# Kernel optimization log

Hardware: AMD Instinct MI355X
Metric: run time of the kernel (lower is better)

Reference implementation:

```python
import jax, jax.numpy as jnp
import numpy as np

B, T, H = 2, 2048, 1024
NH = 16
D = H // NH  # head_dim = 64
SCALE = D ** -0.5


def setup_inputs() -> dict:
    key = jax.random.key(0)
    ks = jax.random.split(key, 10)
    s_in = 1.0 / np.sqrt(H)   # torch Linear init scale for fan_in=H
    s_d = 1.0 / np.sqrt(D)
    return {
        "x":  jax.random.normal(ks[0], (B, T, H), jnp.float32),
        # stacked per-head Q/K projections: [NH, H, D] weights, [NH, D] biases
        "Wq": jax.random.uniform(ks[1], (NH, H, D), jnp.float32, -s_in, s_in),
        "bq": jax.random.uniform(ks[2], (NH, D), jnp.float32, -s_in, s_in),
        "Wk": jax.random.uniform(ks[3], (NH, H, D), jnp.float32, -s_in, s_in),
        "bk": jax.random.uniform(ks[4], (NH, D), jnp.float32, -s_in, s_in),
        # shared V projection H->D
        "Wv": jax.random.uniform(ks[5], (H, D), jnp.float32, -s_in, s_in),
        "bv": jax.random.uniform(ks[6], (D,), jnp.float32, -s_in, s_in),
        # out projection D->H
        "Wo": jax.random.uniform(ks[7], (D, H), jnp.float32, -s_d, s_d),
        "bo": jax.random.uniform(ks[8], (H,), jnp.float32, -s_d, s_d),
    }


def reference(x, Wq, bq, Wk, bk, Wv, bv, Wo, bo):
    # shared value projection: [B,T,D]
    v = jnp.einsum('bth,hd->btd', x, Wv) + bv
    # batched per-head Q/K projections: [NH,B,T,D]
    q = jnp.einsum('bth,nhd->nbtd', x, Wq) + bq[:, None, None, :]
    k = jnp.einsum('bth,nhd->nbtd', x, Wk) + bk[:, None, None, :]
    # scaled causal attention scores: [NH,B,T,T]
    scores = jnp.einsum('nbtd,nbsd->nbts', q, k) * SCALE
    causal = jnp.triu(jnp.ones((T, T), bool), k=1)  # True above diagonal
    scores = jnp.where(causal, -jnp.inf, scores)
    weights = jax.nn.softmax(scores, axis=-1)  # dropout is identity in eval
    # shared V attended per head, then mean over heads: [B,T,D]
    mean_head = jnp.einsum('nbts,bsd->btd', weights, v) / NH
    out = jnp.einsum('btd,dh->bth', mean_head, Wo) + bo
    mean_weights = jnp.mean(weights, axis=0)  # [B,T,T]
    return out, mean_weights
```

## Files before the change

kernel.cpp:

```cpp
#include <hip/hip_runtime.h>
#include <hip/hip_bf16.h>

#define B_ 2
#define T_ 2048
#define H_ 1024
#define NH_ 16
#define D_ 64
#define BT_ (B_*T_)
#define SCALE_ 0.125f
#define LOG2E_ 1.4426950408889634f

typedef _Float16 f16x8 __attribute__((ext_vector_type(8)));
typedef float f32x4 __attribute__((ext_vector_type(4)));

#define MFMA(a,b,c) __builtin_amdgcn_mfma_f32_16x16x32_f16((a),(b),(c),0,0,0)
#define EXP2(x) __builtin_amdgcn_exp2f(x)

typedef const __attribute__((address_space(1))) void GV;
typedef __attribute__((address_space(3))) void LV;

__device__ __forceinline__ size_t toff(int r, int c, int C) {
    return (size_t)((r >> 4) * (C >> 5) + (c >> 5)) * 512 + (size_t)(((c & 31) >> 3) * 128 + (r & 15) * 8 + (c & 7));
}
__device__ __forceinline__ f16x8 frag_ld(const _Float16* base, int rt, int kc, int Cc, int l15, int quad) {
    return *(const f16x8*)(base + (size_t)(rt * Cc + kc) * 512 + quad * 128 + l15 * 8);
}
__device__ __forceinline__ int fbase(int p) {
    int m = p >> 1;
    return (p & 1) ? (m + 1) * (m + 1) : m * m + m;
}

__global__ __launch_bounds__(256) void k_prep(const float* __restrict__ x,
                                              const float* __restrict__ Wq, const float* __restrict__ Wk,
                                              const float* __restrict__ Wv, const float* __restrict__ Wo,
                                              _Float16* __restrict__ xb, _Float16* __restrict__ wqk,
                                              _Float16* __restrict__ wvt, _Float16* __restrict__ wot,
                                              float* __restrict__ mw) {
    int blk = blockIdx.x, tid = threadIdx.x;
    if (blk < 256) {
        const float* xs = x + ((size_t)blk << 14);
        _Float16* dstb = xb + ((size_t)blk << 14);
#pragma unroll
        for (int it = 0; it < 8; it++) {
            int E = it * 2048 + tid * 8;
            int rr = (E >> 3) & 15;
            int h = (E >> 9) * 32 + ((E >> 7) & 3) * 8;
            const float* p = xs + (size_t)rr * 1024 + h;
            float4 f0 = *(const float4*)p;
            float4 f1 = *(const float4*)(p + 4);
            f16x8 o;
            o[0]=(_Float16)f0.x; o[1]=(_Float16)f0.y; o[2]=(_Float16)f0.z; o[3]=(_Float16)f0.w;
            o[4]=(_Float16)f1.x; o[5]=(_Float16)f1.y; o[6]=(_Float16)f1.z; o[7]=(_Float16)f1.w;
            *(f16x8*)(dstb + E) = o;
        }
    } else if (blk < 384) {
        int ct = blk - 256;
        const float* W = (ct < 64) ? Wq : Wk;
        int head = (ct >> 2) & 15;
        int dbase = (ct & 3) * 16;
        _Float16* dstb = wqk + ((size_t)ct << 14);
#pragma unroll
        for (int it = 0; it < 8; it++) {
            int E = it * 2048 + tid * 8;
            int rr = (E >> 3) & 15;
            int h = (E >> 9) * 32 + ((E >> 7) & 3) * 8;
            const float* src = W + (size_t)head * 65536 + (size_t)h * 64 + dbase + rr;
            f16x8 o;
#pragma unroll
            for (int e = 0; e < 8; e++) o[e] = (_Float16)src[(size_t)e * 64];
            *(f16x8*)(dstb + E) = o;
        }
    } else if (blk < 388) {
        int rt = blk - 384;
        _Float16* dstb = wvt + ((size_t)rt << 14);
#pragma unroll
        for (int it = 0; it < 8; it++) {
            int E = it * 2048 + tid * 8;
            int rr = (E >> 3) & 15;
            int h = (E >> 9) * 32 + ((E >> 7) & 3) * 8;
            const float* src = Wv + (size_t)h * 64 + rt * 16 + rr;
            f16x8 o;
#pragma unroll
            for (int e = 0; e < 8; e++) o[e] = (_Float16)src[(size_t)e * 64];
            *(f16x8*)(dstb + E) = o;
        }
    } else if (blk < 392) {
        int bl = blk - 388;
#pragma unroll
        for (int it = 0; it < 8; it++) {
            int G = bl * 16384 + it * 2048 + tid * 8;
            int rt = G >> 10;
            int rem = G & 1023;
            int rr = (rem >> 3) & 15;
            int dd = (rem >> 9) * 32 + ((rem >> 7) & 3) * 8;
            const float* src = Wo + (size_t)dd * 1024 + rt * 16 + rr;
            f16x8 o;
#pragma unroll
            for (int e = 0; e < 8; e++) o[e] = (_Float16)src[(size_t)e * 1024];
            *(f16x8*)(wot + G) = o;
        }
    } else {
        int iz = blk - 392;
        int b = (iz >= 496) ? 1 : 0;
        int i = iz - b * 496;
        int s64 = (int)((sqrtf(8.f * i + 1.f) + 1.f) * 0.5f);
        if (s64 * (s64 - 1) / 2 > i) s64--;
        if ((s64 + 1) * s64 / 2 <= i) s64++;
        int q64 = i - s64 * (s64 - 1) / 2;
        float4 z = {0.f, 0.f, 0.f, 0.f};
#pragma unroll
        for (int it = 0; it < 4; it++) {
            int idx = it * 256 + tid;
            int r = idx >> 4, c4 = idx & 15;
            *(float4*)&mw[(size_t)(b * T_ + q64 * 64 + r) * T_ + s64 * 64 + c4 * 4] = z;
        }
    }
}

__global__ __launch_bounds__(256) void k_gemm(const _Float16* __restrict__ xb, const _Float16* __restrict__ wqk,
                                              const float* __restrict__ bq, const float* __restrict__ bk,
                                              const _Float16* __restrict__ wvt, const float* __restrict__ bv,
                                              _Float16* __restrict__ qh, _Float16* __restrict__ kh,
                                              _Float16* __restrict__ vt) {
    __shared__ __align__(16) unsigned char smem[32768];
    _Float16* As = (_Float16*)smem;
    _Float16* Bs = (_Float16*)(smem + 16384);
    int tid = threadIdx.x, w = tid >> 6, lane = tid & 63, l15 = lane & 15, quad = lane >> 4;
    if (blockIdx.x >= 512) {
        float (*red)[16][64] = (float(*)[16][64])smem;
        int rt = blockIdx.x - 512;
        f32x4 acc[4];
#pragma unroll
        for (int j = 0; j < 4; j++) acc[j] = (f32x4){0.f, 0.f, 0.f, 0.f};
        for (int q = 0; q < 8; q++) {
            int kc = w * 8 + q;
            f16x8 a = frag_ld(xb, rt, kc, 32, l15, quad);
#pragma unroll
            for (int j = 0; j < 4; j++) {
                f16x8 bb = frag_ld(wvt, j, kc, 32, l15, quad);
                acc[j] = MFMA(a, bb, acc[j]);
            }
        }
#pragma unroll
        for (int j = 0; j < 4; j++)
#pragma unroll
            for (int r = 0; r < 4; r++) red[w][quad * 4 + r][j * 16 + l15] = acc[j][r];
        __syncthreads();
        int r = tid >> 4, dg = tid & 15;
        int b = rt >> 7, tt = (rt & 127) * 16 + r;
        _Float16* vtb = vt + (size_t)b * 131072;
#pragma unroll
        for (int e = 0; e < 4; e++) {
            int d = dg * 4 + e;
            float s = red[0][r][d] + red[1][r][d] + red[2][r][d] + red[3][r][d] + bv[d];
            vtb[toff(d, tt, 2048)] = (_Float16)s;
        }
        return;
    }
    int bm = blockIdx.x >> 4, bn = blockIdx.x & 15;
    int rowbase = (w >> 1) * 64, colbase = (w & 1) * 64;
    f32x4 acc[4][4];
#pragma unroll
    for (int i = 0; i < 4; i++)
#pragma unroll
        for (int j = 0; j < 4; j++) acc[i][j] = (f32x4){0.f, 0.f, 0.f, 0.f};

    for (int kk = 0; kk < 16; kk++) {
        __syncthreads();
#pragma unroll
        for (int p = 0; p < 4; p++) {
            int c = w * 4 + p;
            __builtin_amdgcn_global_load_lds((GV*)(xb  + ((size_t)((bm * 8 + (c >> 1)) * 32 + kk * 2 + (c & 1))) * 512 + lane * 8),
                                             (LV*)(As + c * 512 + lane * 8), 16, 0, 0);
            __builtin_amdgcn_global_load_lds((GV*)(wqk + ((size_t)((bn * 8 + (c >> 1)) * 32 + kk * 2 + (c & 1))) * 512 + lane * 8),
                                             (LV*)(Bs + c * 512 + lane * 8), 16, 0, 0);
        }
        __syncthreads();
#pragma unroll
        for (int kc = 0; kc < 2; kc++) {
            f16x8 a[4], bf[4];
#pragma unroll
            for (int i = 0; i < 4; i++) a[i]  = *(const f16x8*)&As[((rowbase >> 4) + i) * 1024 + kc * 512 + quad * 128 + l15 * 8];
#pragma unroll
            for (int j = 0; j < 4; j++) bf[j] = *(const f16x8*)&Bs[((colbase >> 4) + j) * 1024 + kc * 512 + quad * 128 + l15 * 8];
#pragma unroll
            for (int i = 0; i < 4; i++)
#pragma unroll
                for (int j = 0; j < 4; j++) acc[i][j] = MFMA(a[i], bf[j], acc[i][j]);
        }
    }
    __syncthreads();
    int b = (bm * 128) >> 11;
    int t_base = (bm * 128) & 2047;
    int rtbase = (t_base + rowbase) >> 4;
    bool isq = (bn < 8);
    int c2base = isq ? (bn * 128 + colbase) : (bn * 128 + colbase - 1024);
    int n = c2base >> 6;
    _Float16* dst = (isq ? qh : kh) + (size_t)(n * 2 + b) * 131072;
    const float* bias_p = isq ? bq : bk;
    float qs = SCALE_ * LOG2E_;
    int i2 = lane >> 4, rowrb = lane & 15;
#pragma unroll
    for (int j = 0; j < 4; j++) {
        float bias = bias_p[c2base + j * 16 + l15];
        _Float16* stg = ((j & 1) ? Bs : As) + w * 1024;
#pragma unroll
        for (int i = 0; i < 4; i++)
#pragma unroll
            for (int r = 0; r < 4; r++) {
                float v = acc[i][j][r] + bias;
                if (isq) v *= qs;
                stg[(i * 16 + quad * 4 + r) * 16 + l15] = (_Float16)v;
            }
#pragma unroll
        for (int oct = 0; oct < 2; oct++) {
            f16x8 val = *(const f16x8*)&stg[(i2 * 16 + rowrb) * 16 + oct * 8];
            int dd0 = j * 16 + oct * 8;
            *(f16x8*)(dst + (size_t)((rtbase + i2) * 2 + (dd0 >> 5)) * 512 + ((dd0 & 31) >> 3) * 128 + rowrb * 8) = val;
        }
    }
}

__global__ __launch_bounds__(256) void k_pass1(const _Float16* __restrict__ qh, const _Float16* __restrict__ kh,
                                               float* __restrict__ lstat4) {
    int tid = threadIdx.x, w = tid >> 6, lane = tid & 63, l15 = lane & 15, quad = lane >> 4;
    int blk = blockIdx.x;
    int nb = blk & 31;
    int s4 = blk >> 5;
    int n = nb >> 1, b = nb & 1;
    const _Float16* qb = qh + (size_t)(n * 2 + b) * 131072;
    const _Float16* kp = kh + (size_t)(n * 2 + b) * 131072;
    int rt0 = s4 * 4;
    f16x8 aq[4][2];
#pragma unroll
    for (int i = 0; i < 4; i++)
#pragma unroll
        for (int kk = 0; kk < 2; kk++) aq[i][kk] = frag_ld(qb, rt0 + i, kk, 2, l15, quad);
    float l[4][4];
#pragma unroll
    for (int i = 0; i < 4; i++)
#pragma unroll
        for (int r = 0; r < 4; r++) l[i][r] = 0.f;
    int total = 4 * s4 + 4;
    int st_lo = (w * total) >> 2;
    int st_hi = ((w + 1) * total) >> 2;
    for (int st = st_lo; st < st_hi; st++) {
        f16x8 c0 = frag_ld(kp, st, 0, 2, l15, quad);
        f16x8 c1 = frag_ld(kp, st, 1, 2, l15, quad);
#pragma unroll
        for (int i = 0; i < 4; i++) {
            if (st > rt0 + i) continue;
            f32x4 sc = (f32x4){0.f, 0.f, 0.f, 0.f};
            sc = MFMA(aq[i][0], c0, sc);
            sc = MFMA(aq[i][1], c1, sc);
            if (st == rt0 + i) {
#pragma unroll
                for (int r = 0; r < 4; r++)
                    if (l15 <= quad * 4 + r) l[i][r] += EXP2(sc[r]);
            } else {
#pragma unroll
                for (int r = 0; r < 4; r++) l[i][r] += EXP2(sc[r]);
            }
        }
    }
#pragma unroll
    for (int off = 1; off < 16; off <<= 1)
#pragma unroll
        for (int i = 0; i < 4; i++)
#pragma unroll
            for (int r = 0; r < 4; r++) l[i][r] += __shfl_xor(l[i][r], off, 64);
    if (l15 == 0) {
        int base = (n * 2 + b) * 2048 + s4 * 64;
#pragma unroll
        for (int i = 0; i < 4; i++)
#pragma unroll
            for (int r = 0; r < 4; r++)
                lstat4[(size_t)(base + i * 16 + quad * 4 + r) * 4 + w] = l[i][r];
    }
}

__global__ __launch_bounds__(256, 4) void k_pass2(const _Float16* __restrict__ qh, const _Float16* __restrict__ kh,
                                                  const float* __restrict__ lstat4,
                                                  float* __restrict__ mw, _Float16* __restrict__ mwh) {
    __shared__ float sl[16][64];
    __shared__ __align__(16) _Float16 kst[2][8192];
    int blk = blockIdx.x;
    int b = (blk >= 272) ? 1 : 0;
    int i0 = blk - 272 * b;
    int i = (i0 & 7) * 34 + (i0 >> 3);
    int p = 2 * (int)sqrtf((float)i);
    if (p > 31) p = 31;
    while (fbase(p) > i) p--;
    while (p < 31 && fbase(p + 1) <= i) p++;
    int s128 = i - fbase(p);
    int tid = threadIdx.x, w = tid >> 6, lane = tid & 63, l15 = lane & 15, quad = lane >> 4;
    for (int ii = tid; ii < 1024; ii += 256) {
        int h = ii >> 6, r = ii & 63;
        const float4 pl = *(const float4*)&lstat4[(size_t)((h * 2 + b) * 2048 + p * 64 + r) * 4];
        sl[h][r] = -(__log2f(pl.x + pl.y + pl.z + pl.w) + 4.0f);
    }
    int rw = w * 16;
    int rt0 = p * 4 + w;
    int st0 = s128 * 8;
    f32x4 macc[8];
#pragma unroll
    for (int j = 0; j < 8; j++) macc[j] = (f32x4){0.f, 0.f, 0.f, 0.f};

    {
        const _Float16* kp = kh + (size_t)b * 131072;
#pragma unroll
        for (int inst = 0; inst < 4; inst++) {
            int c = inst * 4 + w;
            int gc = (st0 + (c >> 1)) * 2 + (c & 1);
            __builtin_amdgcn_global_load_lds((GV*)(kp + (size_t)gc * 512 + lane * 8),
                                             (LV*)(kst[0] + c * 512 + lane * 8), 16, 0, 0);
        }
    }
    __syncthreads();

    for (int n = 0; n < NH_; n++) {
        if (n < NH_ - 1) {
            const _Float16* kp = kh + (size_t)((n + 1) * 2 + b) * 131072;
#pragma unroll
            for (int inst = 0; inst < 4; inst++) {
                int c = inst * 4 + w;
                int gc = (st0 + (c >> 1)) * 2 + (c & 1);
                __builtin_amdgcn_global_load_lds((GV*)(kp + (size_t)gc * 512 + lane * 8),
                                                 (LV*)(kst[(n + 1) & 1] + c * 512 + lane * 8), 16, 0, 0);
            }
        }
        const _Float16* qb = qh + (size_t)(n * 2 + b) * 131072;
        f16x8 A0 = frag_ld(qb, rt0, 0, 2, l15, quad);
        f16x8 A1 = frag_ld(qb, rt0, 1, 2, l15, quad);
        f32x4 slv = *(const f32x4*)&sl[n][rw + quad * 4];
        const _Float16* ks = kst[n & 1];
#pragma unroll
        for (int j = 0; j < 8; j++) {
            int s64j = 2 * s128 + (j >> 2);
            if (s64j > p) continue;
            f16x8 K0 = *(const f16x8*)&ks[(j * 2 + 0) * 512 + quad * 128 + l15 * 8];
            f16x8 K1 = *(const f16x8*)&ks[(j * 2 + 1) * 512 + quad * 128 + l15 * 8];
            f32x4 sc = slv;
            sc = MFMA(A0, K0, sc);
            sc = MFMA(A1, K1, sc);
            if (s64j == p) {
                int sg = s128 * 128 + j * 16 + l15;
#pragma unroll
                for (int r = 0; r < 4; r++) {
                    int tg = p * 64 + rw + quad * 4 + r;
                    macc[j][r] += (sg <= tg) ? EXP2(sc[r]) : 0.f;
                }
            } else {
#pragma unroll
                for (int r = 0; r < 4; r++) macc[j][r] += EXP2(sc[r]);
            }
        }
        __syncthreads();
    }
    float* mwb = mw + (size_t)b * T_ * T_;
#pragma unroll
    for (int j = 0; j < 8; j++) {
        if (2 * s128 + (j >> 2) > p) continue;
#pragma unroll
        for (int r = 0; r < 4; r++) {
            int tg = p * 64 + rw + quad * 4 + r;
            int sg = s128 * 128 + j * 16 + l15;
            mwb[(size_t)tg * T_ + sg] = macc[j][r];
        }
    }
    _Float16* mhb = mwh + (size_t)b * 4194304;
    _Float16* ws16 = kst[0] + w * 1024;
    int rowrb = lane & 15, qc = lane >> 4;
#pragma unroll
    for (int cc = 0; cc < 4; cc++) {
        if (2 * s128 + (cc >> 1) > p) continue;
#pragma unroll
        for (int j2 = 0; j2 < 2; j2++)
#pragma unroll
            for (int r = 0; r < 4; r++) {
                int clw = j2 * 16 + l15;
                ws16[(clw >> 3) * 128 + (quad * 4 + r) * 8 + (clw & 7)] = (_Float16)macc[cc * 2 + j2][r];
            }
        f16x8 val = *(const f16x8*)&ws16[qc * 128 + rowrb * 8];
        *(f16x8*)(mhb + (size_t)(rt0 * 64 + (s128 * 4 + cc)) * 512 + qc * 128 + rowrb * 8) = val;
    }
}

__global__ __launch_bounds__(512) void k_pass3(const _Float16* __restrict__ mwh, const _Float16* __restrict__ vt,
                                               const _Float16* __restrict__ wot, const float* __restrict__ bo,
                                               float* __restrict__ out0) {
    __shared__ float red[8][16][64];
    __shared__ __align__(16) _Float16 mhs[1024];
    int tid = threadIdx.x, w = tid >> 6, lane = tid & 63, l15 = lane & 15, quad = lane >> 4;
    int blk = blockIdx.x;
    int b = blk & 1;
    int rtb = 127 - (blk >> 1);
    const _Float16* mb = mwh + (size_t)b * 4194304;
    const _Float16* vb = vt + (size_t)b * 131072;
    int nkc = (rtb * 16 + 47) >> 5;
    f32x4 acc[4];
#pragma unroll
    for (int j = 0; j < 4; j++) acc[j] = (f32x4){0.f, 0.f, 0.f, 0.f};
    for (int kc = w; kc < nkc; kc += 8) {
        f16x8 a = frag_ld(mb, rtb, kc, 64, l15, quad);
#pragma unroll
        for (int j = 0; j < 4; j++) {
            f16x8 bb = frag_ld(vb, j, kc, 64, l15, quad);
            acc[j] = MFMA(a, bb, acc[j]);
        }
    }
#pragma unroll
    for (int j = 0; j < 4; j++)
#pragma unroll
        for (int r = 0; r < 4; r++) red[w][quad * 4 + r][j * 16 + l15] = acc[j][r];
    __syncthreads();
    for (int ii = tid; ii < 1024; ii += 512) {
        int r = ii >> 6, d = ii & 63;
        float s = red[0][r][d] + red[1][r][d] + red[2][r][d] + red[3][r][d]
                + red[4][r][d] + red[5][r][d] + red[6][r][d] + red[7][r][d];
        mhs[(d >> 5) * 512 + ((d & 31) >> 3) * 128 + r * 8 + (d & 7)] = (_Float16)s;
    }
    __syncthreads();
    f16x8 A0 = frag_ld(mhs, 0, 0, 2, l15, quad);
    f16x8 A1 = frag_ld(mhs, 0, 1, 2, l15, quad);
    f32x4 acc2[8];
#pragma unroll
    for (int j = 0; j < 8; j++) {
        int ct = w * 8 + j;
        f16x8 b0 = frag_ld(wot, ct, 0, 2, l15, quad);
        f16x8 b1 = frag_ld(wot, ct, 1, 2, l15, quad);
        f32x4 z = (f32x4){0.f, 0.f, 0.f, 0.f};
        z = MFMA(A0, b0, z);
        z = MFMA(A1, b1, z);
        acc2[j] = z;
    }
    int rowb = (b * 128 + rtb) * 16 + quad * 4;
#pragma unroll
    for (int j = 0; j < 8; j++)
#pragma unroll
        for (int r = 0; r < 4; r++) {
            int col = w * 128 + j * 16 + l15;
            out0[(size_t)(rowb + r) * 1024 + col] = acc2[j][r] + bo[col];
        }
}

extern "C" void kernel_launch(void* const* d_in, const int* in_sizes, int n_in,
                              void* d_out, int out_size, void* d_ws, size_t ws_size,
                              hipStream_t stream) {
    const float* x  = (const float*)d_in[0];
    const float* Wq = (const float*)d_in[1];
    const float* bq = (const float*)d_in[2];
    const float* Wk = (const float*)d_in[3];
    const float* bk = (const float*)d_in[4];
    const float* Wv = (const float*)d_in[5];
    const float* bv = (const float*)d_in[6];
    const float* Wo = (const float*)d_in[7];
    const float* bo = (const float*)d_in[8];
    char* ws = (char*)d_ws;
    _Float16* xb    = (_Float16*)(ws + 0);
    _Float16* wqk   = (_Float16*)(ws + 8388608);
    _Float16* wvt   = (_Float16*)(ws + 12582912);
    _Float16* mwh   = (_Float16*)(ws + 0);
    _Float16* qh    = (_Float16*)(ws + 16777216);
    _Float16* kh    = (_Float16*)(ws + 25165824);
    _Float16* vt    = (_Float16*)(ws + 33554432);
    float*    lstat4= (float*)   (ws + 34078720);
    _Float16* wot   = (_Float16*)(ws + 39321600);
    float* out0 = (float*)d_out;
    float* mw   = out0 + (size_t)BT_ * H_;

    k_prep   <<<1384, 256, 0, stream>>>(x, Wq, Wk, Wv, Wo, xb, wqk, wvt, wot, mw);
    k_gemm   <<<768,  256, 0, stream>>>(xb, wqk, bq, bk, wvt, bv, qh, kh, vt);
    k_pass1  <<<1024, 256, 0, stream>>>(qh, kh, lstat4);
    k_pass2  <<<544,  256, 0, stream>>>(qh, kh, lstat4, mw, mwh);
    k_pass3  <<<256,  512, 0, stream>>>(mwh, vt, wot, bo, out0);
}
```

Measured before the change: 189.8 us.

## Pipeline QK projection GEMM with triple-buffered LDS and move V projection into pass1

The QK projection GEMM now uses 512-thread blocks with a 256x128 tile, a three-stage LDS ring filled by global_load_lds, and prefetch loads spread across four MFMA sub-steps separated by barriers. It also adds a block-index swizzle and MFMA priority raising. The small V projection blocks move out of the GEMM launch and are appended to k_pass1's grid. This is meant to hide global-memory latency and balance the GEMM grid, at the cost of one block per CU and hand-tuned vmcnt waits that must match the load count.

```diff
diff --git a/kernel.cpp b/kernel.cpp
--- a/kernel.cpp
+++ b/kernel.cpp
@@ -117,83 +117,144 @@
     }
 }
 
-__global__ __launch_bounds__(256) void k_gemm(const _Float16* __restrict__ xb, const _Float16* __restrict__ wqk,
-                                              const float* __restrict__ bq, const float* __restrict__ bk,
-                                              const _Float16* __restrict__ wvt, const float* __restrict__ bv,
-                                              _Float16* __restrict__ qh, _Float16* __restrict__ kh,
-                                              _Float16* __restrict__ vt) {
-    __shared__ __align__(16) unsigned char smem[32768];
-    _Float16* As = (_Float16*)smem;
-    _Float16* Bs = (_Float16*)(smem + 16384);
+__device__ __forceinline__ void stage_a(const _Float16* xb, _Float16* dst, int bm, int t, int li, int w, int lane) {
+    int c = li * 8 + w;
+    __builtin_amdgcn_global_load_lds((GV*)(xb + ((size_t)((bm * 16 + (c >> 1)) * 32 + t * 2 + (c & 1))) * 512 + lane * 8),
+                                     (LV*)(dst + c * 512 + lane * 8), 16, 0, 0);
+}
+__device__ __forceinline__ void stage_b(const _Float16* wqk, _Float16* dst, int bn, int t, int li, int w, int lane) {
+    int c = li * 8 + w;
+    __builtin_amdgcn_global_load_lds((GV*)(wqk + ((size_t)((bn * 8 + (c >> 1)) * 32 + t * 2 + (c & 1))) * 512 + lane * 8),
+                                     (LV*)(dst + c * 512 + lane * 8), 16, 0, 0);
+}
+
+__global__ __launch_bounds__(512, 1) void k_gemm(const _Float16* __restrict__ xb, const _Float16* __restrict__ wqk,
+                                                 const float* __restrict__ bq, const float* __restrict__ bk,
+                                                 _Float16* __restrict__ qh, _Float16* __restrict__ kh) {
+    __shared__ __align__(16) _Float16 sA[3][16384];
+    __shared__ __align__(16) _Float16 sB[3][8192];
     int tid = threadIdx.x, w = tid >> 6, lane = tid & 63, l15 = lane & 15, quad = lane >> 4;
-    if (blockIdx.x >= 512) {
-        float (*red)[16][64] = (float(*)[16][64])smem;
-        int rt = blockIdx.x - 512;
-        f32x4 acc[4];
-#pragma unroll
-        for (int j = 0; j < 4; j++) acc[j] = (f32x4){0.f, 0.f, 0.f, 0.f};
-        for (int q = 0; q < 8; q++) {
-            int kc = w * 8 + q;
-            f16x8 a = frag_ld(xb, rt, kc, 32, l15, quad);
-#pragma unroll
-            for (int j = 0; j < 4; j++) {
-                f16x8 bb = frag_ld(wvt, j, kc, 32, l15, quad);
-                acc[j] = MFMA(a, bb, acc[j]);
-            }
-        }
-#pragma unroll
-        for (int j = 0; j < 4; j++)
-#pragma unroll
-            for (int r = 0; r < 4; r++) red[w][quad * 4 + r][j * 16 + l15] = acc[j][r];
-        __syncthreads();
-        int r = tid >> 4, dg = tid & 15;
-        int b = rt >> 7, tt = (rt & 127) * 16 + r;
-        _Float16* vtb = vt + (size_t)b * 131072;
-#pragma unroll
-        for (int e = 0; e < 4; e++) {
-            int d = dg * 4 + e;
-            float s = red[0][r][d] + red[1][r][d] + red[2][r][d] + red[3][r][d] + bv[d];
-            vtb[toff(d, tt, 2048)] = (_Float16)s;
-        }
-        return;
-    }
-    int bm = blockIdx.x >> 4, bn = blockIdx.x & 15;
-    int rowbase = (w >> 1) * 64, colbase = (w & 1) * 64;
+    int bid = blockIdx.x;
+    int swz = (bid & 7) * 32 + (bid >> 3);
+    int bm = swz >> 4, bn = swz & 15;
+    int wr = w >> 1, wc = w & 1;
+    int qoff = quad * 128 + l15 * 8;
     f32x4 acc[4][4];
 #pragma unroll
     for (int i = 0; i < 4; i++)
 #pragma unroll
         for (int j = 0; j < 4; j++) acc[i][j] = (f32x4){0.f, 0.f, 0.f, 0.f};
 
-    for (int kk = 0; kk < 16; kk++) {
-        __syncthreads();
-#pragma unroll
-        for (int p = 0; p < 4; p++) {
-            int c = w * 4 + p;
-            __builtin_amdgcn_global_load_lds((GV*)(xb  + ((size_t)((bm * 8 + (c >> 1)) * 32 + kk * 2 + (c & 1))) * 512 + lane * 8),
-                                             (LV*)(As + c * 512 + lane * 8), 16, 0, 0);
-            __builtin_amdgcn_global_load_lds((GV*)(wqk + ((size_t)((bn * 8 + (c >> 1)) * 32 + kk * 2 + (c & 1))) * 512 + lane * 8),
-                                             (LV*)(Bs + c * 512 + lane * 8), 16, 0, 0);
-        }
-        __syncthreads();
-#pragma unroll
-        for (int kc = 0; kc < 2; kc++) {
-            f16x8 a[4], bf[4];
-#pragma unroll
-            for (int i = 0; i < 4; i++) a[i]  = *(const f16x8*)&As[((rowbase >> 4) + i) * 1024 + kc * 512 + quad * 128 + l15 * 8];
-#pragma unroll
-            for (int j = 0; j < 4; j++) bf[j] = *(const f16x8*)&Bs[((colbase >> 4) + j) * 1024 + kc * 512 + quad * 128 + l15 * 8];
-#pragma unroll
-            for (int i = 0; i < 4; i++)
-#pragma unroll
-                for (int j = 0; j < 4; j++) acc[i][j] = MFMA(a[i], bf[j], acc[i][j]);
-        }
+#pragma unroll
+    for (int li = 0; li < 4; li++) stage_a(xb, sA[0], bm, 0, li, w, lane);
+#pragma unroll
+    for (int li = 0; li < 2; li++) stage_b(wqk, sB[0], bn, 0, li, w, lane);
+#pragma unroll
+    for (int li = 0; li < 4; li++) stage_a(xb, sA[1], bm, 1, li, w, lane);
+#pragma unroll
+    for (int li = 0; li < 2; li++) stage_b(wqk, sB[1], bn, 1, li, w, lane);
+    asm volatile("s_waitcnt vmcnt(6)" ::: "memory");
+    __builtin_amdgcn_s_barrier();
+
+#pragma unroll 1
+    for (int t = 0; t < 16; t++) {
+        int bi = t % 3, pi = (t + 2) % 3;
+        const _Float16* A = sA[bi];
+        const _Float16* Bp = sB[bi];
+        bool pref = (t + 2 < 16);
+        if (pref) { stage_a(xb, sA[pi], bm, t + 2, 0, w, lane); stage_a(xb, sA[pi], bm, t + 2, 1, w, lane); }
+        {
+            f16x8 a[2][2], bf[2][2];
+#pragma unroll
+            for (int ii = 0; ii < 2; ii++)
+#pragma unroll
+                for (int kc = 0; kc < 2; kc++) a[ii][kc] = *(const f16x8*)&A[((wr * 4 + ii) * 2 + kc) * 512 + qoff];
+#pragma unroll
+            for (int jj = 0; jj < 2; jj++)
+#pragma unroll
+                for (int kc = 0; kc < 2; kc++) bf[jj][kc] = *(const f16x8*)&Bp[((wc * 4 + jj) * 2 + kc) * 512 + qoff];
+            __builtin_amdgcn_s_setprio(1);
+#pragma unroll
+            for (int ii = 0; ii < 2; ii++)
+#pragma unroll
+                for (int jj = 0; jj < 2; jj++)
+#pragma unroll
+                    for (int kc = 0; kc < 2; kc++) acc[ii][jj] = MFMA(a[ii][kc], bf[jj][kc], acc[ii][jj]);
+            __builtin_amdgcn_s_setprio(0);
+        }
+        __builtin_amdgcn_s_barrier();
+        if (pref) { stage_a(xb, sA[pi], bm, t + 2, 2, w, lane); stage_a(xb, sA[pi], bm, t + 2, 3, w, lane); }
+        {
+            f16x8 a[2][2], bf[2][2];
+#pragma unroll
+            for (int ii = 0; ii < 2; ii++)
+#pragma unroll
+                for (int kc = 0; kc < 2; kc++) a[ii][kc] = *(const f16x8*)&A[((wr * 4 + ii) * 2 + kc) * 512 + qoff];
+#pragma unroll
+            for (int jj = 0; jj < 2; jj++)
+#pragma unroll
+                for (int kc = 0; kc < 2; kc++) bf[jj][kc] = *(const f16x8*)&Bp[((wc * 4 + 2 + jj) * 2 + kc) * 512 + qoff];
+            __builtin_amdgcn_s_setprio(1);
+#pragma unroll
+            for (int ii = 0; ii < 2; ii++)
+#pragma unroll
+                for (int jj = 0; jj < 2; jj++)
+#pragma unroll
+                    for (int kc = 0; kc < 2; kc++) acc[ii][2 + jj] = MFMA(a[ii][kc], bf[jj][kc], acc[ii][2 + jj]);
+            __builtin_amdgcn_s_setprio(0);
+        }
+        __builtin_amdgcn_s_barrier();
+        if (pref) stage_b(wqk, sB[pi], bn, t + 2, 0, w, lane);
+        {
+            f16x8 a[2][2], bf[2][2];
+#pragma unroll
+            for (int ii = 0; ii < 2; ii++)
+#pragma unroll
+                for (int kc = 0; kc < 2; kc++) a[ii][kc] = *(const f16x8*)&A[((wr * 4 + 2 + ii) * 2 + kc) * 512 + qoff];
+#pragma unroll
+            for (int jj = 0; jj < 2; jj++)
+#pragma unroll
+                for (int kc = 0; kc < 2; kc++) bf[jj][kc] = *(const f16x8*)&Bp[((wc * 4 + jj) * 2 + kc) * 512 + qoff];
+            __builtin_amdgcn_s_setprio(1);
+#pragma unroll
+            for (int ii = 0; ii < 2; ii++)
+#pragma unroll
+                for (int jj = 0; jj < 2; jj++)
+#pragma unroll
+                    for (int kc = 0; kc < 2; kc++) acc[2 + ii][jj] = MFMA(a[ii][kc], bf[jj][kc], acc[2 + ii][jj]);
+            __builtin_amdgcn_s_setprio(0);
+        }
+        __builtin_amdgcn_s_barrier();
+        if (pref) stage_b(wqk, sB[pi], bn, t + 2, 1, w, lane);
+        {
+            f16x8 a[2][2], bf[2][2];
+#pragma unroll
+            for (int ii = 0; ii < 2; ii++)
+#pragma unroll
+                for (int kc = 0; kc < 2; kc++) a[ii][kc] = *(const f16x8*)&A[((wr * 4 + 2 + ii) * 2 + kc) * 512 + qoff];
+#pragma unroll
+            for (int jj = 0; jj < 2; jj++)
+#pragma unroll
+                for (int kc = 0; kc < 2; kc++) bf[jj][kc] = *(const f16x8*)&Bp[((wc * 4 + 2 + jj) * 2 + kc) * 512 + qoff];
+            __builtin_amdgcn_s_setprio(1);
+#pragma unroll
+            for (int ii = 0; ii < 2; ii++)
+#pragma unroll
+                for (int jj = 0; jj < 2; jj++)
+#pragma unroll
+                    for (int kc = 0; kc < 2; kc++) acc[2 + ii][2 + jj] = MFMA(a[ii][kc], bf[jj][kc], acc[2 + ii][2 + jj]);
+            __builtin_amdgcn_s_setprio(0);
+        }
+        if (pref) asm volatile("s_waitcnt vmcnt(6)" ::: "memory");
+        else      asm volatile("s_waitcnt vmcnt(0)" ::: "memory");
+        __builtin_amdgcn_s_barrier();
     }
     __syncthreads();
-    int b = (bm * 128) >> 11;
-    int t_base = (bm * 128) & 2047;
-    int rtbase = (t_base + rowbase) >> 4;
+    int b = (bm * 256) >> 11;
+    int t_base = (bm * 256) & 2047;
+    int rtbase = (t_base + wr * 64) >> 4;
     bool isq = (bn < 8);
+    int colbase = wc * 64;
     int c2base = isq ? (bn * 128 + colbase) : (bn * 128 + colbase - 1024);
     int n = c2base >> 6;
     _Float16* dst = (isq ? qh : kh) + (size_t)(n * 2 + b) * 131072;
@@ -203,7 +264,7 @@
 #pragma unroll
     for (int j = 0; j < 4; j++) {
         float bias = bias_p[c2base + j * 16 + l15];
-        _Float16* stg = ((j & 1) ? Bs : As) + w * 1024;
+        _Float16* stg = sA[0] + ((j & 1) ? 8192 : 0) + w * 1024;
 #pragma unroll
         for (int i = 0; i < 4; i++)
 #pragma unroll
@@ -222,9 +283,42 @@
 }
 
 __global__ __launch_bounds__(256) void k_pass1(const _Float16* __restrict__ qh, const _Float16* __restrict__ kh,
-                                               float* __restrict__ lstat4) {
+                                               float* __restrict__ lstat4,
+                                               const _Float16* __restrict__ xb, const _Float16* __restrict__ wvt,
+                                               const float* __restrict__ bv, _Float16* __restrict__ vt) {
+    __shared__ float red[4][16][64];
     int tid = threadIdx.x, w = tid >> 6, lane = tid & 63, l15 = lane & 15, quad = lane >> 4;
     int blk = blockIdx.x;
+    if (blk >= 1024) {
+        int rt = blk - 1024;
+        f32x4 acc[4];
+#pragma unroll
+        for (int j = 0; j < 4; j++) acc[j] = (f32x4){0.f, 0.f, 0.f, 0.f};
+        for (int q = 0; q < 8; q++) {
+            int kc = w * 8 + q;
+            f16x8 a = frag_ld(xb, rt, kc, 32, l15, quad);
+#pragma unroll
+            for (int j = 0; j < 4; j++) {
+                f16x8 bb = frag_ld(wvt, j, kc, 32, l15, quad);
+                acc[j] = MFMA(a, bb, acc[j]);
+            }
+        }
+#pragma unroll
+        for (int j = 0; j < 4; j++)
+#pragma unroll
+            for (int r = 0; r < 4; r++) red[w][quad * 4 + r][j * 16 + l15] = acc[j][r];
+        __syncthreads();
+        int r = tid >> 4, dg = tid & 15;
+        int b = rt >> 7, tt = (rt & 127) * 16 + r;
+        _Float16* vtb = vt + (size_t)b * 131072;
+#pragma unroll
+        for (int e = 0; e < 4; e++) {
+            int d = dg * 4 + e;
+            float s = red[0][r][d] + red[1][r][d] + red[2][r][d] + red[3][r][d] + bv[d];
+            vtb[toff(d, tt, 2048)] = (_Float16)s;
+        }
+        return;
+    }
     int nb = blk & 31;
     int s4 = blk >> 5;
     int n = nb >> 1, b = nb & 1;
@@ -470,8 +564,8 @@
     float* mw   = out0 + (size_t)BT_ * H_;
 
     k_prep   <<<1384, 256, 0, stream>>>(x, Wq, Wk, Wv, Wo, xb, wqk, wvt, wot, mw);
-    k_gemm   <<<768,  256, 0, stream>>>(xb, wqk, bq, bk, wvt, bv, qh, kh, vt);
-    k_pass1  <<<1024, 256, 0, stream>>>(qh, kh, lstat4);
+    k_gemm   <<<256,  512, 0, stream>>>(xb, wqk, bq, bk, qh, kh);
+    k_pass1  <<<1280, 256, 0, stream>>>(qh, kh, lstat4, xb, wvt, bv, vt);
     k_pass2  <<<544,  256, 0, stream>>>(qh, kh, lstat4, mw, mwh);
     k_pass3  <<<256,  512, 0, stream>>>(mwh, vt, wot, bo, out0);
 }
```

Measured after the change: 199.8 us. +5.3%, slower.
